# Optimization experiments

Hardware: AMD Instinct MI355X
Metric: run time of the kernel (lower is better)

The kernel has to match this reference:

```python
import jax, jax.numpy as jnp
import numpy as np

L, B, T, C, H = 8, 2, 1024, 1024, 16
DH = C // H          # 64, head dim (even, required for RoPE)
DFF = 4 * C          # 4096
THETA = 10000.0
EPS = 1e-5


def _ln(x, scale, bias):
    m = jnp.mean(x, axis=-1, keepdims=True)
    v = jnp.mean((x - m) ** 2, axis=-1, keepdims=True)
    return (x - m) * jax.lax.rsqrt(v + EPS) * scale + bias


def _rope_cos_sin():
    # matches precompute_freqs_cis: freqs_cis[t, j] = exp(i * t * theta^{-2j/dim})
    inv = 1.0 / (THETA ** (jnp.arange(0, DH, 2, dtype=jnp.float32) / DH))  # (DH/2,)
    ang = jnp.arange(T, dtype=jnp.float32)[:, None] * inv[None, :]         # (T, DH/2)
    return jnp.cos(ang), jnp.sin(ang)


def _apply_rope(x, cos, sin):
    # x: (B,H,T,DH); complex multiply on interleaved pairs == torch.view_as_complex path
    xr = x.reshape(B, H, T, DH // 2, 2)
    x0, x1 = xr[..., 0], xr[..., 1]
    o0 = x0 * cos - x1 * sin
    o1 = x0 * sin + x1 * cos
    return jnp.stack([o0, o1], axis=-1).reshape(B, H, T, DH)


def setup_inputs() -> dict:
    key = jax.random.key(0)
    ks = jax.random.split(key, 20)
    s = 0.02
    p = lambda k, shape: (jax.random.normal(k, shape, jnp.float32) * s)
    return {
        "x": jax.random.normal(ks[0], (B, T, C), jnp.float32),
        "Wq": p(ks[1], (L, C, C)), "bq": jnp.zeros((L, C), jnp.float32),
        "Wk": p(ks[2], (L, C, C)), "bk": jnp.zeros((L, C), jnp.float32),
        "Wv": p(ks[3], (L, C, C)), "bv": jnp.zeros((L, C), jnp.float32),
        "Wo": p(ks[4], (L, C, C)), "bo": jnp.zeros((L, C), jnp.float32),
        "ln1_s": jnp.ones((L, C), jnp.float32), "ln1_b": jnp.zeros((L, C), jnp.float32),
        "ln2_s": jnp.ones((L, C), jnp.float32), "ln2_b": jnp.zeros((L, C), jnp.float32),
        "W1": p(ks[5], (L, C, DFF)), "b1": jnp.zeros((L, DFF), jnp.float32),
        "W2": p(ks[6], (L, DFF, C)), "b2": jnp.zeros((L, C), jnp.float32),
        "lnf_s": jnp.ones((C,), jnp.float32), "lnf_b": jnp.zeros((C,), jnp.float32),
    }


def reference(x, Wq, bq, Wk, bk, Wv, bv, Wo, bo,
              ln1_s, ln1_b, ln2_s, ln2_b, W1, b1, W2, b2, lnf_s, lnf_b):
    cos, sin = _rope_cos_sin()
    causal = jnp.tril(jnp.ones((T, T), bool))
    inv_sqrt_dh = jnp.float32(1.0 / np.sqrt(DH))

    def layer(h, p):
        wq, bq_, wk, bk_, wv, bv_, wo, bo_, s1, c1, s2, c2, w1, d1, w2, d2 = p
        a = _ln(h, s1, c1)
        q = (a @ wq + bq_).reshape(B, T, H, DH).transpose(0, 2, 1, 3)  # (B,H,T,DH)
        k = (a @ wk + bk_).reshape(B, T, H, DH).transpose(0, 2, 1, 3)
        v = (a @ wv + bv_).reshape(B, T, H, DH).transpose(0, 2, 1, 3)
        q = _apply_rope(q, cos, sin)
        k = _apply_rope(k, cos, sin)
        att = jnp.einsum('bhqd,bhkd->bhqk', q, k) * inv_sqrt_dh
        att = jnp.where(causal, att, -jnp.inf)
        att = jax.nn.softmax(att, axis=-1)
        y = jnp.einsum('bhqk,bhkd->bhqd', att, v)
        y = y.transpose(0, 2, 1, 3).reshape(B, T, C)
        h = h + (y @ wo + bo_)
        m = _ln(h, s2, c2)
        h = h + (jax.nn.gelu(m @ w1 + d1, approximate=False) @ w2 + d2)
        return h, None

    h, _ = jax.lax.scan(
        layer, x,
        (Wq, bq, Wk, bk, Wv, bv, Wo, bo, ln1_s, ln1_b, ln2_s, ln2_b, W1, b1, W2, b2))
    return _ln(h, lnf_s, lnf_b)
```

## Files before the change

kernel.cpp:

```cpp
#include <hip/hip_runtime.h>
#include <cstdint>
#include <cstddef>

#define L_   8
#define B_   2
#define T_   1024
#define C_   1024
#define H_   16
#define DH_  64
#define DFF_ 4096
#define M_   2048

typedef __attribute__((ext_vector_type(4))) float f32x4;
typedef __attribute__((ext_vector_type(8))) short short8_t;
typedef __attribute__((ext_vector_type(8))) __bf16 bf16x8_t;
typedef __attribute__((ext_vector_type(4))) unsigned short ushort4_t;

__device__ __forceinline__ float bf2f(unsigned short u) {
  unsigned int i = ((unsigned int)u) << 16;
  return __builtin_bit_cast(float, i);
}
__device__ __forceinline__ unsigned short f2bf(float f) {
  unsigned int u = __builtin_bit_cast(unsigned int, f);
  u += 0x7fff + ((u >> 16) & 1);
  return (unsigned short)(u >> 16);
}
__device__ __forceinline__ f32x4 mfma16x16x32(short8_t a, short8_t b, f32x4 c) {
  return __builtin_amdgcn_mfma_f32_16x16x32_bf16(
      __builtin_bit_cast(bf16x8_t, a), __builtin_bit_cast(bf16x8_t, b), c, 0, 0, 0);
}
__device__ __forceinline__ void async_copy16(const void* g, void* l) {
  __builtin_amdgcn_global_load_lds(
      (const __attribute__((address_space(1))) unsigned int*)g,
      (__attribute__((address_space(3))) unsigned int*)l, 16, 0, 0);
}

template<int OUTF32>
__global__ __launch_bounds__(256) void ln_k(const float* __restrict__ X,
                                            const float* __restrict__ gam,
                                            const float* __restrict__ bet,
                                            void* __restrict__ out) {
  const int row = blockIdx.x;
  const int tid = threadIdx.x;
  const int lane = tid & 63, w = tid >> 6;
  const float4 v = ((const float4*)(X + (size_t)row * C_))[tid];
  float sum = v.x + v.y + v.z + v.w;
  float sq  = v.x*v.x + v.y*v.y + v.z*v.z + v.w*v.w;
#pragma unroll
  for (int d = 1; d < 64; d <<= 1) {
    sum += __shfl_xor(sum, d, 64);
    sq  += __shfl_xor(sq,  d, 64);
  }
  __shared__ float red[8];
  if (lane == 0) { red[w] = sum; red[4 + w] = sq; }
  __syncthreads();
  sum = red[0] + red[1] + red[2] + red[3];
  sq  = red[4] + red[5] + red[6] + red[7];
  const float mean = sum * (1.0f / C_);
  const float var  = sq * (1.0f / C_) - mean * mean;
  const float inv  = rsqrtf(var + 1e-5f);
  const int col = tid * 4;
  const float xs[4] = { v.x, v.y, v.z, v.w };
  if (OUTF32) {
    float4 ov;
    ov.x = (xs[0]-mean)*inv*gam[col+0] + bet[col+0];
    ov.y = (xs[1]-mean)*inv*gam[col+1] + bet[col+1];
    ov.z = (xs[2]-mean)*inv*gam[col+2] + bet[col+2];
    ov.w = (xs[3]-mean)*inv*gam[col+3] + bet[col+3];
    ((float4*)((float*)out + (size_t)row * C_))[tid] = ov;
  } else {
    ushort4_t ov;
#pragma unroll
    for (int i = 0; i < 4; ++i)
      ov[i] = f2bf((xs[i]-mean)*inv*gam[col+i] + bet[col+i]);
    *(ushort4_t*)((unsigned short*)out + (size_t)row * C_ + col) = ov;
  }
}

__global__ __launch_bounds__(256) void transpose_bf(const float* __restrict__ W,
                                                    unsigned short* __restrict__ Wt,
                                                    int R, int Cc) {
  __shared__ float tile[32][33];
  const int c0 = blockIdx.x * 32, r0 = blockIdx.y * 32;
  const int tx = threadIdx.x & 31, ty = threadIdx.x >> 5;
#pragma unroll
  for (int i = 0; i < 4; ++i)
    tile[ty + 8*i][tx] = W[(size_t)(r0 + ty + 8*i) * Cc + c0 + tx];
  __syncthreads();
#pragma unroll
  for (int i = 0; i < 4; ++i)
    Wt[(size_t)(c0 + ty + 8*i) * R + r0 + tx] = f2bf(tile[tx][ty + 8*i]);
}

template<int EPI>
__global__ __launch_bounds__(256) void gemm64(
    const unsigned short* __restrict__ A,
    const unsigned short* __restrict__ Bt,
    const float* __restrict__ bias0,
    const float* __restrict__ bias1,
    const float* __restrict__ bias2,
    void* __restrict__ out0, void* __restrict__ out1, void* __restrict__ out2,
    int M, int N, int K) {
  __shared__ __align__(16) unsigned short As[64 * 32];
  __shared__ __align__(16) unsigned short Bs[128 * 32];
  const int tid = threadIdx.x;
  const int lane = tid & 63;
  const int w = tid >> 6;
  const int ln15 = lane & 15, lg = lane >> 4;
  const int row0 = blockIdx.y * 64, col0 = blockIdx.x * 128;
  const int wr = w >> 1, wc = w & 1;

  const int kper = K / gridDim.z;
  const int k0 = blockIdx.z * kper;

  f32x4 acc[2][4] = {};

  const int rA  = tid >> 2,          ccA = (tid & 3) * 8;
  const int rB0 = tid >> 2,          ccB = (tid & 3) * 8;
  const int rB1 = (256 + tid) >> 2;

  for (int kt = k0; kt < k0 + kper; kt += 32) {
    async_copy16(A  + (size_t)(row0 + rA)  * K + kt + ccA, (char*)As + ((size_t)w * 64) * 16);
    async_copy16(Bt + (size_t)(col0 + rB0) * K + kt + ccB, (char*)Bs + ((size_t)w * 64) * 16);
    async_copy16(Bt + (size_t)(col0 + rB1) * K + kt + ccB, (char*)Bs + ((size_t)(256 + w * 64)) * 16);
    __syncthreads();
    short8_t af[2], bfr[4];
#pragma unroll
    for (int m = 0; m < 2; ++m)
      af[m] = *(const short8_t*)(As + (wr*32 + m*16 + ln15) * 32 + lg * 8);
#pragma unroll
    for (int n = 0; n < 4; ++n)
      bfr[n] = *(const short8_t*)(Bs + (wc*64 + n*16 + ln15) * 32 + lg * 8);
#pragma unroll
    for (int m = 0; m < 2; ++m)
#pragma unroll
      for (int n = 0; n < 4; ++n)
        acc[m][n] = mfma16x16x32(af[m], bfr[n], acc[m][n]);
    __syncthreads();
  }

#pragma unroll
  for (int m = 0; m < 2; ++m) {
#pragma unroll
    for (int n = 0; n < 4; ++n) {
#pragma unroll
      for (int r = 0; r < 4; ++r) {
        const int rg = row0 + wr*32 + m*16 + lg*4 + r;
        const int cg = col0 + wc*64 + n*16 + ln15;
        float v = acc[m][n][r];
        if (EPI == 0) {
          if (cg < 1024) {
            v += bias0[cg];
            ((unsigned short*)out0)[(size_t)rg * C_ + cg] = f2bf(v);
          } else if (cg < 2048) {
            v += bias1[cg - 1024];
            ((unsigned short*)out1)[(size_t)rg * C_ + (cg - 1024)] = f2bf(v);
          } else {
            const int ch = cg - 2048;
            v += bias2[ch];
            const int hh = ch >> 6, dh = ch & 63;
            const int bb = rg >> 10, t = rg & 1023;
            ((unsigned short*)out2)[(((size_t)(bb * H_ + hh) * DH_ + dh) << 10) + t] = f2bf(v);
          }
        } else if (EPI == 2) {
          v += bias0[cg];
          v = 0.5f * v * (1.0f + erff(v * 0.70710678118654752f));
          ((unsigned short*)out0)[(size_t)rg * N + cg] = f2bf(v);
        } else {
          ((float*)out0)[((size_t)blockIdx.z * M_ + rg) * (size_t)N + cg] = v;
        }
      }
    }
  }
}

template<int NS>
__global__ __launch_bounds__(256) void reduce_k(float* __restrict__ h,
                                                const float* __restrict__ bias,
                                                const float* __restrict__ part) {
  const size_t idx = (size_t)blockIdx.x * 256 + threadIdx.x;
  const size_t i4 = idx * 4;
  const int colg = (int)(i4 & (C_ - 1)) >> 2;
  float4 acc = ((float4*)h)[idx];
  const float4 b = ((const float4*)bias)[colg];
  acc.x += b.x; acc.y += b.y; acc.z += b.z; acc.w += b.w;
#pragma unroll
  for (int z = 0; z < NS; ++z) {
    const float4 p = ((const float4*)(part + (size_t)z * M_ * C_))[idx];
    acc.x += p.x; acc.y += p.y; acc.z += p.z; acc.w += p.w;
  }
  ((float4*)h)[idx] = acc;
}

__global__ __launch_bounds__(256) void rope_k(unsigned short* __restrict__ Q,
                                              unsigned short* __restrict__ Kb) {
  const size_t p = (size_t)blockIdx.x * 256 + threadIdx.x;
  unsigned short* ptr = blockIdx.y ? Kb : Q;
  const int cpair = (int)(p & 511);
  const int t = (int)((p >> 9) & 1023);
  const int j = cpair & 31;
  const float ang = (float)t * expf((float)j * -0.28782313662425572f);
  float cs, sn;
  sincosf(ang, &sn, &cs);
  unsigned int u = *(unsigned int*)(ptr + 2 * p);
  const float x0 = bf2f((unsigned short)(u & 0xffff));
  const float x1 = bf2f((unsigned short)(u >> 16));
  const float o0 = x0 * cs - x1 * sn;
  const float o1 = x0 * sn + x1 * cs;
  *(unsigned int*)(ptr + 2 * p) = (unsigned int)f2bf(o0) | ((unsigned int)f2bf(o1) << 16);
}

template<bool MASK>
__device__ __forceinline__ void attn_tile(
    const int kb, const int ln15, const int lg, const int rowg0,
    const unsigned short* __restrict__ Kp,
    const unsigned short* __restrict__ Vp,
    const short8_t aq0, const short8_t aq1,
    float* __restrict__ m_run, float* __restrict__ l_run,
    f32x4* __restrict__ o, unsigned short* __restrict__ P) {
  const unsigned short* kt = Kp + (size_t)kb * 64 * C_;
  const unsigned short* vt = Vp + kb * 64;
  short8_t bk[4][2], vb[2][4];
#pragma unroll
  for (int n = 0; n < 4; ++n) {
    bk[n][0] = *(const short8_t*)(kt + (size_t)n * 16 * C_);
    bk[n][1] = *(const short8_t*)(kt + (size_t)n * 16 * C_ + 32);
  }
  f32x4 s[4] = {};
#pragma unroll
  for (int n = 0; n < 4; ++n) {
    s[n] = mfma16x16x32(aq0, bk[n][0], s[n]);
    s[n] = mfma16x16x32(aq1, bk[n][1], s[n]);
  }
#pragma unroll
  for (int c = 0; c < 2; ++c)
#pragma unroll
    for (int n = 0; n < 4; ++n)
      vb[c][n] = *(const short8_t*)(vt + (size_t)n * 16 * T_ + c * 32);

  const float SCL = 0.18033688011116012f;
  float mx[4];
#pragma unroll
  for (int r = 0; r < 4; ++r) {
    float mr = -1e30f;
#pragma unroll
    for (int n = 0; n < 4; ++n) {
      float v = s[n][r] * SCL;
      if (MASK && (kb * 64 + n * 16 + ln15) > (rowg0 + r)) v = -1e30f;
      s[n][r] = v;
      mr = fmaxf(mr, v);
    }
    mx[r] = mr;
  }
#pragma unroll
  for (int d = 1; d < 16; d <<= 1)
#pragma unroll
    for (int r = 0; r < 4; ++r) mx[r] = fmaxf(mx[r], __shfl_xor(mx[r], d, 64));
#pragma unroll
  for (int r = 0; r < 4; ++r) {
    const float mn = fmaxf(m_run[r], mx[r]);
    const float scf = exp2f(m_run[r] - mn);
    m_run[r] = mn;
    float rs = 0.0f;
#pragma unroll
    for (int n = 0; n < 4; ++n) {
      const float pv = exp2f(s[n][r] - mn);
      s[n][r] = pv;
      rs += pv;
    }
#pragma unroll
    for (int d = 1; d < 16; d <<= 1) rs += __shfl_xor(rs, d, 64);
    l_run[r] = l_run[r] * scf + rs;
#pragma unroll
    for (int n = 0; n < 4; ++n) o[n][r] *= scf;
  }
  __syncthreads();
#pragma unroll
  for (int r = 0; r < 4; ++r)
#pragma unroll
    for (int n = 0; n < 4; ++n)
      P[(lg * 4 + r) * 64 + n * 16 + ln15] = f2bf(s[n][r]);
  __syncthreads();
#pragma unroll
  for (int c = 0; c < 2; ++c) {
    const short8_t pa = *(const short8_t*)(P + ln15 * 64 + c * 32 + lg * 8);
#pragma unroll
    for (int n = 0; n < 4; ++n)
      o[n] = mfma16x16x32(pa, vb[c][n], o[n]);
  }
}

__global__ __launch_bounds__(64) void attn_k(const unsigned short* __restrict__ Q,
                                             const unsigned short* __restrict__ Kb,
                                             const unsigned short* __restrict__ Vt,
                                             unsigned short* __restrict__ Y) {
  __shared__ __align__(16) unsigned short P[16 * 64];
  const int lane = threadIdx.x;
  const int ln15 = lane & 15, lg = lane >> 4;
  const int qt = blockIdx.x, bh = blockIdx.y;
  const int b = bh >> 4, h = bh & 15;
  const int q0 = qt * 16;

  short8_t aq0, aq1;
  {
    const unsigned short* qp = Q + ((size_t)(b * T_ + q0 + ln15)) * C_ + h * DH_ + lg * 8;
    aq0 = *(const short8_t*)(qp);
    aq1 = *(const short8_t*)(qp + 32);
  }
  float m_run[4] = { -1e30f, -1e30f, -1e30f, -1e30f };
  float l_run[4] = {};
  f32x4 o[4] = {};
  const int rowg0 = q0 + lg * 4;
  const unsigned short* Kp = Kb + ((size_t)b * T_ + ln15) * C_ + h * DH_ + lg * 8;
  const unsigned short* Vp = Vt + ((size_t)bh * DH_ + ln15) * T_ + lg * 8;

  const int kb_last = qt >> 2;
  for (int kb = 0; kb < kb_last; ++kb)
    attn_tile<false>(kb, ln15, lg, rowg0, Kp, Vp, aq0, aq1, m_run, l_run, o, P);
  attn_tile<true>(kb_last, ln15, lg, rowg0, Kp, Vp, aq0, aq1, m_run, l_run, o, P);

#pragma unroll
  for (int n = 0; n < 4; ++n)
#pragma unroll
    for (int r = 0; r < 4; ++r) {
      const float val = o[n][r] / l_run[r];
      Y[((size_t)(b * T_ + rowg0 + r)) * C_ + h * DH_ + n * 16 + ln15] = f2bf(val);
    }
}

extern "C" void kernel_launch(void* const* d_in, const int* in_sizes, int n_in,
                              void* d_out, int out_size, void* d_ws, size_t ws_size,
                              hipStream_t stream) {
  const float* x    = (const float*)d_in[0];
  const float* Wq   = (const float*)d_in[1];
  const float* bq   = (const float*)d_in[2];
  const float* Wk   = (const float*)d_in[3];
  const float* bk   = (const float*)d_in[4];
  const float* Wv   = (const float*)d_in[5];
  const float* bv   = (const float*)d_in[6];
  const float* Wo   = (const float*)d_in[7];
  const float* bo   = (const float*)d_in[8];
  const float* ln1s = (const float*)d_in[9];
  const float* ln1b = (const float*)d_in[10];
  const float* ln2s = (const float*)d_in[11];
  const float* ln2b = (const float*)d_in[12];
  const float* W1   = (const float*)d_in[13];
  const float* b1   = (const float*)d_in[14];
  const float* W2   = (const float*)d_in[15];
  const float* b2   = (const float*)d_in[16];
  const float* lnfs = (const float*)d_in[17];
  const float* lnfb = (const float*)d_in[18];

  const size_t MB = (size_t)1 << 20;
  char* ws = (char*)d_ws;
  float*          h      = (float*)(ws + 0);
  unsigned short* a_bf   = (unsigned short*)(ws + 8*MB);
  unsigned short* q_bf   = (unsigned short*)(ws + 12*MB);
  unsigned short* k_bf   = (unsigned short*)(ws + 16*MB);
  unsigned short* vt_bf  = (unsigned short*)(ws + 20*MB);
  unsigned short* y_bf   = (unsigned short*)(ws + 24*MB);
  unsigned short* mid_bf = (unsigned short*)(ws + 28*MB);
  unsigned short* wt_bf  = (unsigned short*)(ws + 44*MB);
  float*          part   = (float*)(ws + 52*MB);

  hipMemcpyAsync(h, x, (size_t)M_ * C_ * sizeof(float), hipMemcpyDeviceToDevice, stream);

  for (int l = 0; l < L_; ++l) {
    const size_t wOff = (size_t)l * C_ * C_;
    const size_t fOff = (size_t)l * C_ * DFF_;
    ln_k<0><<<M_, 256, 0, stream>>>(h, ln1s + l*C_, ln1b + l*C_, a_bf);
    transpose_bf<<<dim3(32, 32), 256, 0, stream>>>(Wq + wOff, wt_bf,           C_, C_);
    transpose_bf<<<dim3(32, 32), 256, 0, stream>>>(Wk + wOff, wt_bf + C_*C_,   C_, C_);
    transpose_bf<<<dim3(32, 32), 256, 0, stream>>>(Wv + wOff, wt_bf + 2*C_*C_, C_, C_);
    gemm64<0><<<dim3(24, 32, 1), 256, 0, stream>>>(a_bf, wt_bf,
        bq + l*C_, bk + l*C_, bv + l*C_, q_bf, k_bf, vt_bf, M_, 3*C_, C_);
    rope_k<<<dim3((B_*T_*C_/2)/256, 2), 256, 0, stream>>>(q_bf, k_bf);
    attn_k<<<dim3(T_/16, B_*H_), 64, 0, stream>>>(q_bf, k_bf, vt_bf, y_bf);
    transpose_bf<<<dim3(32, 32), 256, 0, stream>>>(Wo + wOff, wt_bf, C_, C_);
    gemm64<3><<<dim3(8, 32, 2), 256, 0, stream>>>(y_bf, wt_bf,
        nullptr, nullptr, nullptr, part, nullptr, nullptr, M_, C_, C_);
    reduce_k<2><<<(M_*C_/4)/256, 256, 0, stream>>>(h, bo + l*C_, part);
    ln_k<0><<<M_, 256, 0, stream>>>(h, ln2s + l*C_, ln2b + l*C_, a_bf);
    transpose_bf<<<dim3(128, 32), 256, 0, stream>>>(W1 + fOff, wt_bf, C_, DFF_);
    gemm64<2><<<dim3(32, 32, 1), 256, 0, stream>>>(a_bf, wt_bf,
        b1 + l*DFF_, nullptr, nullptr, mid_bf, nullptr, nullptr, M_, DFF_, C_);
    transpose_bf<<<dim3(32, 128), 256, 0, stream>>>(W2 + fOff, wt_bf, DFF_, C_);
    gemm64<3><<<dim3(8, 32, 4), 256, 0, stream>>>(mid_bf, wt_bf,
        nullptr, nullptr, nullptr, part, nullptr, nullptr, M_, C_, DFF_);
    reduce_k<4><<<(M_*C_/4)/256, 256, 0, stream>>>(h, b2 + l*C_, part);
  }
  ln_k<1><<<M_, 256, 0, stream>>>(h, lnfs, lnfb, d_out);
}
```

Baseline: 1.846 ms.

## Batch weight conversion, fuse RoPE into QKV epilogue, fuse residual reduce with LayerNorm

All per-layer weight transposes and bf16 conversions are replaced by one up-front conversion kernel covering every layer. RoPE is folded into the QKV GEMM epilogue using a lane shuffle, which removes a separate pass over Q and K. Each residual reduction is merged with the following LayerNorm, and the FFN1 GEMM gets its own 128x128 tile kernel with a fused GELU. Together these cut kernel launch count and global memory traffic, at the cost of a larger weight workspace and more transcendental math in the GEMM epilogue.

```diff
diff --git a/kernel.cpp b/kernel.cpp
--- a/kernel.cpp
+++ b/kernel.cpp
@@ -35,11 +35,48 @@
       (__attribute__((address_space(3))) unsigned int*)l, 16, 0, 0);
 }
 
-template<int OUTF32>
+__global__ __launch_bounds__(256) void convert_k(
+    const float* __restrict__ Wq, const float* __restrict__ Wk,
+    const float* __restrict__ Wv, const float* __restrict__ Wo,
+    const float* __restrict__ W1, const float* __restrict__ W2,
+    unsigned short* __restrict__ wt) {
+  __shared__ float tile[32][33];
+  const int bx = blockIdx.x;
+  const int layer = bx / 12288;
+  const int r = bx - layer * 12288;
+  const float* src; unsigned short* dst; int R, Cc, t;
+  unsigned short* wl = wt + (size_t)layer * 12582912;
+  if (r < 3072) {
+    const int mat = r >> 10; t = r & 1023;
+    src = (mat == 0 ? Wq : mat == 1 ? Wk : Wv) + (size_t)layer * 1048576;
+    dst = wl + (size_t)mat * 1048576; R = 1024; Cc = 1024;
+  } else if (r < 4096) {
+    t = r - 3072; src = Wo + (size_t)layer * 1048576;
+    dst = wl + 3145728; R = 1024; Cc = 1024;
+  } else if (r < 8192) {
+    t = r - 4096; src = W1 + (size_t)layer * 4194304;
+    dst = wl + 4194304; R = 1024; Cc = 4096;
+  } else {
+    t = r - 8192; src = W2 + (size_t)layer * 4194304;
+    dst = wl + 8388608; R = 4096; Cc = 1024;
+  }
+  const int nTc = Cc >> 5;
+  const int tr = t / nTc, tc = t - tr * nTc;
+  const int r0 = tr * 32, c0 = tc * 32;
+  const int tx = threadIdx.x & 31, ty = threadIdx.x >> 5;
+#pragma unroll
+  for (int i = 0; i < 4; ++i)
+    tile[ty + 8*i][tx] = src[(size_t)(r0 + ty + 8*i) * Cc + c0 + tx];
+  __syncthreads();
+#pragma unroll
+  for (int i = 0; i < 4; ++i)
+    dst[(size_t)(c0 + ty + 8*i) * R + r0 + tx] = f2bf(tile[tx][ty + 8*i]);
+}
+
 __global__ __launch_bounds__(256) void ln_k(const float* __restrict__ X,
                                             const float* __restrict__ gam,
                                             const float* __restrict__ bet,
-                                            void* __restrict__ out) {
+                                            unsigned short* __restrict__ out) {
   const int row = blockIdx.x;
   const int tid = threadIdx.x;
   const int lane = tid & 63, w = tid >> 6;
@@ -61,35 +98,66 @@
   const float inv  = rsqrtf(var + 1e-5f);
   const int col = tid * 4;
   const float xs[4] = { v.x, v.y, v.z, v.w };
-  if (OUTF32) {
+  ushort4_t ov;
+#pragma unroll
+  for (int i = 0; i < 4; ++i)
+    ov[i] = f2bf((xs[i]-mean)*inv*gam[col+i] + bet[col+i]);
+  *(ushort4_t*)(out + (size_t)row * C_ + col) = ov;
+}
+
+template<int NS, int FINAL>
+__global__ __launch_bounds__(256) void reduce_ln(
+    float* __restrict__ h, const float* __restrict__ bias,
+    const float* __restrict__ part,
+    const float* __restrict__ gam, const float* __restrict__ bet,
+    void* __restrict__ out) {
+  const int row = blockIdx.x;
+  const int tid = threadIdx.x;
+  const int lane = tid & 63, w = tid >> 6;
+  const size_t base = (size_t)row * C_;
+  float4 v = ((const float4*)(h + base))[tid];
+  const float4 b = ((const float4*)bias)[tid];
+  v.x += b.x; v.y += b.y; v.z += b.z; v.w += b.w;
+#pragma unroll
+  for (int z = 0; z < NS; ++z) {
+    const float4 p = ((const float4*)(part + (size_t)z * M_ * C_ + base))[tid];
+    v.x += p.x; v.y += p.y; v.z += p.z; v.w += p.w;
+  }
+  if (!FINAL) ((float4*)(h + base))[tid] = v;
+  float sum = v.x + v.y + v.z + v.w;
+  float sq  = v.x*v.x + v.y*v.y + v.z*v.z + v.w*v.w;
+#pragma unroll
+  for (int d = 1; d < 64; d <<= 1) {
+    sum += __shfl_xor(sum, d, 64);
+    sq  += __shfl_xor(sq,  d, 64);
+  }
+  __shared__ float red[8];
+  if (lane == 0) { red[w] = sum; red[4 + w] = sq; }
+  __syncthreads();
+  sum = red[0] + red[1] + red[2] + red[3];
+  sq  = red[4] + red[5] + red[6] + red[7];
+  const float mean = sum * (1.0f / C_);
+  const float var  = sq * (1.0f / C_) - mean * mean;
+  const float inv  = rsqrtf(var + 1e-5f);
+  const float4 g  = ((const float4*)gam)[tid];
+  const float4 be = ((const float4*)bet)[tid];
+  if (FINAL) {
     float4 ov;
-    ov.x = (xs[0]-mean)*inv*gam[col+0] + bet[col+0];
-    ov.y = (xs[1]-mean)*inv*gam[col+1] + bet[col+1];
-    ov.z = (xs[2]-mean)*inv*gam[col+2] + bet[col+2];
-    ov.w = (xs[3]-mean)*inv*gam[col+3] + bet[col+3];
-    ((float4*)((float*)out + (size_t)row * C_))[tid] = ov;
+    ov.x = (v.x-mean)*inv*g.x + be.x;
+    ov.y = (v.y-mean)*inv*g.y + be.y;
+    ov.z = (v.z-mean)*inv*g.z + be.z;
+    ov.w = (v.w-mean)*inv*g.w + be.w;
+    ((float4*)out)[(size_t)row * 256 + tid] = ov;
   } else {
     ushort4_t ov;
+    const float xs[4] = { v.x, v.y, v.z, v.w };
+    const float gs[4] = { g.x, g.y, g.z, g.w };
+    const float bs[4] = { be.x, be.y, be.z, be.w };
 #pragma unroll
     for (int i = 0; i < 4; ++i)
-      ov[i] = f2bf((xs[i]-mean)*inv*gam[col+i] + bet[col+i]);
-    *(ushort4_t*)((unsigned short*)out + (size_t)row * C_ + col) = ov;
-  }
-}
-
-__global__ __launch_bounds__(256) void transpose_bf(const float* __restrict__ W,
-                                                    unsigned short* __restrict__ Wt,
-                                                    int R, int Cc) {
-  __shared__ float tile[32][33];
-  const int c0 = blockIdx.x * 32, r0 = blockIdx.y * 32;
-  const int tx = threadIdx.x & 31, ty = threadIdx.x >> 5;
-#pragma unroll
-  for (int i = 0; i < 4; ++i)
-    tile[ty + 8*i][tx] = W[(size_t)(r0 + ty + 8*i) * Cc + c0 + tx];
-  __syncthreads();
-#pragma unroll
-  for (int i = 0; i < 4; ++i)
-    Wt[(size_t)(c0 + ty + 8*i) * R + r0 + tx] = f2bf(tile[tx][ty + 8*i]);
+      ov[i] = f2bf((xs[i]-mean)*inv*gs[i] + bs[i]);
+    *(ushort4_t*)((unsigned short*)out + base + tid * 4) = ov;
+  }
 }
 
 template<int EPI>
@@ -149,12 +217,18 @@
         const int cg = col0 + wc*64 + n*16 + ln15;
         float v = acc[m][n][r];
         if (EPI == 0) {
-          if (cg < 1024) {
-            v += bias0[cg];
-            ((unsigned short*)out0)[(size_t)rg * C_ + cg] = f2bf(v);
-          } else if (cg < 2048) {
-            v += bias1[cg - 1024];
-            ((unsigned short*)out1)[(size_t)rg * C_ + (cg - 1024)] = f2bf(v);
+          if (cg < 2048) {
+            v += (cg < 1024) ? bias0[cg] : bias1[cg - 1024];
+            const float vp = __shfl_xor(v, 1, 64);
+            const int j = (cg & 63) >> 1;
+            const float ang = (float)(rg & 1023) *
+                              exp2f((float)j * -0.41524101186092029f);
+            float sn, cs;
+            sincosf(ang, &sn, &cs);
+            const float ov = (cg & 1) ? (vp * sn + v * cs) : (v * cs - vp * sn);
+            unsigned short* dstp = (cg < 1024) ? (unsigned short*)out0
+                                               : (unsigned short*)out1;
+            dstp[(size_t)rg * C_ + (cg & 1023)] = f2bf(ov);
           } else {
             const int ch = cg - 2048;
             v += bias2[ch];
@@ -162,10 +236,6 @@
             const int bb = rg >> 10, t = rg & 1023;
             ((unsigned short*)out2)[(((size_t)(bb * H_ + hh) * DH_ + dh) << 10) + t] = f2bf(v);
           }
-        } else if (EPI == 2) {
-          v += bias0[cg];
-          v = 0.5f * v * (1.0f + erff(v * 0.70710678118654752f));
-          ((unsigned short*)out0)[(size_t)rg * N + cg] = f2bf(v);
         } else {
           ((float*)out0)[((size_t)blockIdx.z * M_ + rg) * (size_t)N + cg] = v;
         }
@@ -174,40 +244,61 @@
   }
 }
 
-template<int NS>
-__global__ __launch_bounds__(256) void reduce_k(float* __restrict__ h,
-                                                const float* __restrict__ bias,
-                                                const float* __restrict__ part) {
-  const size_t idx = (size_t)blockIdx.x * 256 + threadIdx.x;
-  const size_t i4 = idx * 4;
-  const int colg = (int)(i4 & (C_ - 1)) >> 2;
-  float4 acc = ((float4*)h)[idx];
-  const float4 b = ((const float4*)bias)[colg];
-  acc.x += b.x; acc.y += b.y; acc.z += b.z; acc.w += b.w;
-#pragma unroll
-  for (int z = 0; z < NS; ++z) {
-    const float4 p = ((const float4*)(part + (size_t)z * M_ * C_))[idx];
-    acc.x += p.x; acc.y += p.y; acc.z += p.z; acc.w += p.w;
-  }
-  ((float4*)h)[idx] = acc;
-}
-
-__global__ __launch_bounds__(256) void rope_k(unsigned short* __restrict__ Q,
-                                              unsigned short* __restrict__ Kb) {
-  const size_t p = (size_t)blockIdx.x * 256 + threadIdx.x;
-  unsigned short* ptr = blockIdx.y ? Kb : Q;
-  const int cpair = (int)(p & 511);
-  const int t = (int)((p >> 9) & 1023);
-  const int j = cpair & 31;
-  const float ang = (float)t * expf((float)j * -0.28782313662425572f);
-  float cs, sn;
-  sincosf(ang, &sn, &cs);
-  unsigned int u = *(unsigned int*)(ptr + 2 * p);
-  const float x0 = bf2f((unsigned short)(u & 0xffff));
-  const float x1 = bf2f((unsigned short)(u >> 16));
-  const float o0 = x0 * cs - x1 * sn;
-  const float o1 = x0 * sn + x1 * cs;
-  *(unsigned int*)(ptr + 2 * p) = (unsigned int)f2bf(o0) | ((unsigned int)f2bf(o1) << 16);
+__global__ __launch_bounds__(256) void gemm128_gelu(
+    const unsigned short* __restrict__ A,
+    const unsigned short* __restrict__ Bt,
+    const float* __restrict__ bias,
+    unsigned short* __restrict__ out,
+    int M, int N, int K) {
+  __shared__ __align__(16) unsigned short As[128 * 32];
+  __shared__ __align__(16) unsigned short Bs[128 * 32];
+  const int tid = threadIdx.x;
+  const int lane = tid & 63;
+  const int w = tid >> 6;
+  const int ln15 = lane & 15, lg = lane >> 4;
+  const int row0 = blockIdx.y * 128, col0 = blockIdx.x * 128;
+  const int wr = w >> 1, wc = w & 1;
+
+  f32x4 acc[4][4] = {};
+
+  const int r0s = tid >> 2,         cc0 = (tid & 3) * 8;
+  const int r1s = (256 + tid) >> 2, cc1 = (tid & 3) * 8;
+
+  for (int kt = 0; kt < K; kt += 32) {
+    async_copy16(A  + (size_t)(row0 + r0s) * K + kt + cc0, (char*)As + ((size_t)w * 64) * 16);
+    async_copy16(A  + (size_t)(row0 + r1s) * K + kt + cc1, (char*)As + ((size_t)(256 + w * 64)) * 16);
+    async_copy16(Bt + (size_t)(col0 + r0s) * K + kt + cc0, (char*)Bs + ((size_t)w * 64) * 16);
+    async_copy16(Bt + (size_t)(col0 + r1s) * K + kt + cc1, (char*)Bs + ((size_t)(256 + w * 64)) * 16);
+    __syncthreads();
+    short8_t af[4], bfr[4];
+#pragma unroll
+    for (int m = 0; m < 4; ++m)
+      af[m] = *(const short8_t*)(As + (wr*64 + m*16 + ln15) * 32 + lg * 8);
+#pragma unroll
+    for (int n = 0; n < 4; ++n)
+      bfr[n] = *(const short8_t*)(Bs + (wc*64 + n*16 + ln15) * 32 + lg * 8);
+#pragma unroll
+    for (int m = 0; m < 4; ++m)
+#pragma unroll
+      for (int n = 0; n < 4; ++n)
+        acc[m][n] = mfma16x16x32(af[m], bfr[n], acc[m][n]);
+    __syncthreads();
+  }
+
+#pragma unroll
+  for (int m = 0; m < 4; ++m) {
+#pragma unroll
+    for (int n = 0; n < 4; ++n) {
+#pragma unroll
+      for (int r = 0; r < 4; ++r) {
+        const int rg = row0 + wr*64 + m*16 + lg*4 + r;
+        const int cg = col0 + wc*64 + n*16 + ln15;
+        float v = acc[m][n][r] + bias[cg];
+        v = 0.5f * v * (1.0f + erff(v * 0.70710678118654752f));
+        out[(size_t)rg * N + cg] = f2bf(v);
+      }
+    }
+  }
 }
 
 template<bool MASK>
@@ -360,34 +451,32 @@
   unsigned short* vt_bf  = (unsigned short*)(ws + 20*MB);
   unsigned short* y_bf   = (unsigned short*)(ws + 24*MB);
   unsigned short* mid_bf = (unsigned short*)(ws + 28*MB);
-  unsigned short* wt_bf  = (unsigned short*)(ws + 44*MB);
-  float*          part   = (float*)(ws + 52*MB);
-
+  float*          part   = (float*)(ws + 44*MB);
+  unsigned short* wt_all = (unsigned short*)(ws + 76*MB);
+
+  convert_k<<<8 * 12288, 256, 0, stream>>>(Wq, Wk, Wv, Wo, W1, W2, wt_all);
   hipMemcpyAsync(h, x, (size_t)M_ * C_ * sizeof(float), hipMemcpyDeviceToDevice, stream);
+  ln_k<<<M_, 256, 0, stream>>>(h, ln1s, ln1b, a_bf);
 
   for (int l = 0; l < L_; ++l) {
-    const size_t wOff = (size_t)l * C_ * C_;
-    const size_t fOff = (size_t)l * C_ * DFF_;
-    ln_k<0><<<M_, 256, 0, stream>>>(h, ln1s + l*C_, ln1b + l*C_, a_bf);
-    transpose_bf<<<dim3(32, 32), 256, 0, stream>>>(Wq + wOff, wt_bf,           C_, C_);
-    transpose_bf<<<dim3(32, 32), 256, 0, stream>>>(Wk + wOff, wt_bf + C_*C_,   C_, C_);
-    transpose_bf<<<dim3(32, 32), 256, 0, stream>>>(Wv + wOff, wt_bf + 2*C_*C_, C_, C_);
-    gemm64<0><<<dim3(24, 32, 1), 256, 0, stream>>>(a_bf, wt_bf,
+    const unsigned short* wt_l = wt_all + (size_t)l * 12582912;
+    gemm64<0><<<dim3(24, 32, 1), 256, 0, stream>>>(a_bf, wt_l,
         bq + l*C_, bk + l*C_, bv + l*C_, q_bf, k_bf, vt_bf, M_, 3*C_, C_);
-    rope_k<<<dim3((B_*T_*C_/2)/256, 2), 256, 0, stream>>>(q_bf, k_bf);
     attn_k<<<dim3(T_/16, B_*H_), 64, 0, stream>>>(q_bf, k_bf, vt_bf, y_bf);
-    transpose_bf<<<dim3(32, 32), 256, 0, stream>>>(Wo + wOff, wt_bf, C_, C_);
-    gemm64<3><<<dim3(8, 32, 2), 256, 0, stream>>>(y_bf, wt_bf,
+    gemm64<3><<<dim3(8, 32, 2), 256, 0, stream>>>(y_bf, wt_l + 3145728,
         nullptr, nullptr, nullptr, part, nullptr, nullptr, M_, C_, C_);
-    reduce_k<2><<<(M_*C_/4)/256, 256, 0, stream>>>(h, bo + l*C_, part);
-    ln_k<0><<<M_, 256, 0, stream>>>(h, ln2s + l*C_, ln2b + l*C_, a_bf);
-    transpose_bf<<<dim3(128, 32), 256, 0, stream>>>(W1 + fOff, wt_bf, C_, DFF_);
-    gemm64<2><<<dim3(32, 32, 1), 256, 0, stream>>>(a_bf, wt_bf,
-        b1 + l*DFF_, nullptr, nullptr, mid_bf, nullptr, nullptr, M_, DFF_, C_);
-    transpose_bf<<<dim3(32, 128), 256, 0, stream>>>(W2 + fOff, wt_bf, DFF_, C_);
-    gemm64<3><<<dim3(8, 32, 4), 256, 0, stream>>>(mid_bf, wt_bf,
+    reduce_ln<2, 0><<<M_, 256, 0, stream>>>(h, bo + l*C_, part,
+        ln2s + l*C_, ln2b + l*C_, a_bf);
+    gemm128_gelu<<<dim3(32, 16), 256, 0, stream>>>(a_bf, wt_l + 4194304,
+        b1 + l*DFF_, mid_bf, M_, DFF_, C_);
+    gemm64<3><<<dim3(8, 32, 4), 256, 0, stream>>>(mid_bf, wt_l + 8388608,
         nullptr, nullptr, nullptr, part, nullptr, nullptr, M_, C_, DFF_);
-    reduce_k<4><<<(M_*C_/4)/256, 256, 0, stream>>>(h, b2 + l*C_, part);
-  }
-  ln_k<1><<<M_, 256, 0, stream>>>(h, lnfs, lnfb, d_out);
-}
+    if (l < L_ - 1) {
+      reduce_ln<4, 0><<<M_, 256, 0, stream>>>(h, b2 + l*C_, part,
+          ln1s + (l+1)*C_, ln1b + (l+1)*C_, a_bf);
+    } else {
+      reduce_ln<4, 1><<<M_, 256, 0, stream>>>(h, b2 + l*C_, part,
+          lnfs, lnfb, d_out);
+    }
+  }
+}
```

Measured after the change: 1.859 ms. About the same (+0.7%).
